# Kernel optimization log

Hardware: AMD Instinct MI355X
Metric: run time of the kernel (lower is better)

The kernel has to match this reference:

```python
import jax, jax.numpy as jnp
import numpy as np

B0 = 4
DIM = 128        # d_model / channels
D_INNER = 256    # expand * dim
D_STATE = 16
D_CONV = 4
DT_RANK = 8      # ceil(dim/16)
NSLICES = 16
IMG = (16, 24, 24)
EPS_LN = 1e-5    # nn.LayerNorm default
EPS_CF = 1e-6    # channels_first LayerNorm eps


def setup_inputs() -> dict:
    key = jax.random.key(0)
    ks = jax.random.split(key, 32)
    rn = lambda k, s, sc=1.0: jax.random.normal(k, s, jnp.float32) * sc
    inp = {"x": rn(ks[0], (B0, DIM) + IMG)}
    inp["ln_w"] = jnp.ones((DIM,), jnp.float32)
    inp["ln_b"] = jnp.zeros((DIM,), jnp.float32)
    inp["in_proj_w"] = rn(ks[1], (2 * D_INNER, DIM), 0.05)
    inp["out_proj_w"] = rn(ks[2], (DIM, D_INNER), 0.05)
    for i, sfx in enumerate(["f", "b", "s"]):
        b = 3 + i * 7
        inp[f"conv_w_{sfx}"] = rn(ks[b], (D_INNER, 1, D_CONV), 0.2)
        inp[f"conv_b_{sfx}"] = rn(ks[b + 1], (D_INNER,), 0.02)
        inp[f"xproj_w_{sfx}"] = rn(ks[b + 2], (DT_RANK + 2 * D_STATE, D_INNER), 0.05)
        inp[f"dtproj_w_{sfx}"] = rn(ks[b + 3], (D_INNER, DT_RANK), 0.1)
        inp[f"dtproj_b_{sfx}"] = rn(ks[b + 4], (D_INNER,), 0.1)
        # S4D-real-style init: A in [1, d_state]
        inp[f"A_log_{sfx}"] = jnp.log(jax.random.uniform(ks[b + 5], (D_INNER, D_STATE), jnp.float32, 1.0, 16.0))
        inp[f"D_{sfx}"] = jnp.ones((D_INNER,), jnp.float32)
    inp["nm_w"] = jnp.ones((DIM,), jnp.float32)
    inp["nm_b"] = jnp.zeros((DIM,), jnp.float32)
    return inp


def _mamba_inner(xz, conv_w, conv_b, xproj_w, dtproj_w, dtproj_b, A_log, Dp):
    """mamba_inner_fn_no_out_proj: xz (B, 2*d_inner, L) -> y (B, d_inner, L)."""
    d = conv_w.shape[0]
    x, z = xz[:, :d], xz[:, d:]
    # causal depthwise conv1d
    xc = jax.lax.conv_general_dilated(
        x, conv_w, (1,), [(conv_w.shape[-1] - 1, 0)],
        dimension_numbers=("NCH", "OIH", "NCH"), feature_group_count=d)
    xc = jax.nn.silu(xc + conv_b[None, :, None])
    x_dbl = jnp.einsum("bdl,rd->brl", xc, xproj_w)  # (B, R+2N, L)
    R = dtproj_w.shape[1]
    N = A_log.shape[1]
    dt = jax.nn.softplus(jnp.einsum("brl,dr->bdl", x_dbl[:, :R], dtproj_w) + dtproj_b[None, :, None])
    Bm, Cm = x_dbl[:, R:R + N], x_dbl[:, R + N:]
    A = -jnp.exp(A_log)  # (d, N)
    seq = (jnp.moveaxis(dt, -1, 0), jnp.moveaxis(xc, -1, 0),
           jnp.moveaxis(Bm, -1, 0), jnp.moveaxis(Cm, -1, 0))
    h0 = jnp.zeros((xz.shape[0], d, N), xz.dtype)

    def step(h, t):
        dt_t, u_t, B_t, C_t = t  # (B,d) (B,d) (B,N) (B,N)
        h = h * jnp.exp(dt_t[..., None] * A) + (dt_t * u_t)[..., None] * B_t[:, None, :]
        return h, jnp.einsum("bdn,bn->bd", h, C_t)

    _, ys = jax.lax.scan(step, h0, seq)  # ys: (L, B, d)
    y = jnp.moveaxis(ys, 0, -1) + Dp[None, :, None] * xc
    return y * jax.nn.silu(z)


def reference(x, ln_w, ln_b, in_proj_w, out_proj_w,
              conv_w_f, conv_b_f, xproj_w_f, dtproj_w_f, dtproj_b_f, A_log_f, D_f,
              conv_w_b, conv_b_b, xproj_w_b, dtproj_w_b, dtproj_b_b, A_log_b, D_b,
              conv_w_s, conv_b_s, xproj_w_s, dtproj_w_s, dtproj_b_s, A_log_s, D_s,
              nm_w, nm_b):
    B, C = x.shape[:2]
    img = x.shape[2:]
    L = int(np.prod(img))
    xf = jnp.transpose(x.reshape(B, C, L), (0, 2, 1))  # (B, L, C)
    # MambaLayer.norm (nn.LayerNorm over C)
    mu = xf.mean(-1, keepdims=True)
    var = ((xf - mu) ** 2).mean(-1, keepdims=True)
    xn = (xf - mu) / jnp.sqrt(var + EPS_LN) * ln_w + ln_b
    xz = jnp.einsum("blc,ec->bel", xn, in_proj_w)  # (B, 2*d_inner, L)
    # forward-direction scan
    out_f = _mamba_inner(xz, conv_w_f, conv_b_f, xproj_w_f, dtproj_w_f, dtproj_b_f, A_log_f, D_f)
    # backward-direction scan on flipped sequence, flipped back
    out_bw = jnp.flip(_mamba_inner(jnp.flip(xz, -1), conv_w_b, conv_b_b, xproj_w_b,
                                   dtproj_w_b, dtproj_b_b, A_log_b, D_b), -1)
    # slice-direction: torch chunk(nslices,-1) -> stack(-1) -> flatten(-2)
    ns, Lns = NSLICES, L // NSLICES
    xz_s = jnp.transpose(xz.reshape(B, 2 * D_INNER, ns, Lns), (0, 1, 3, 2)).reshape(B, 2 * D_INNER, L)
    out_s = _mamba_inner(xz_s, conv_w_s, conv_b_s, xproj_w_s, dtproj_w_s, dtproj_b_s, A_log_s, D_s)
    # torch: reshape(B,-1,ns,L//ns).permute(0,1,3,2).flatten(-2)
    out_s = jnp.transpose(out_s.reshape(B, D_INNER, ns, Lns), (0, 1, 3, 2)).reshape(B, D_INNER, L)
    y = jnp.einsum("bdl,cd->blc", out_f + out_bw + out_s, out_proj_w)  # out_proj, no bias
    x_mamba = jnp.transpose(y, (0, 2, 1)).reshape(x.shape) + x  # MambaLayer residual
    # SMBBlock: channels_first LayerNorm + residual
    mu2 = x_mamba.mean(1, keepdims=True)
    var2 = ((x_mamba - mu2) ** 2).mean(1, keepdims=True)
    bc = (C,) + (1,) * len(img)
    normed = nm_w.reshape(bc) * ((x_mamba - mu2) / jnp.sqrt(var2 + EPS_CF)) + nm_b.reshape(bc)
    return x_mamba + normed
```

## Files before the change

kernel.cpp:

```cpp
#include <hip/hip_runtime.h>

#define LSEQ 9216
#define CDIM 128
#define ED   512
#define DI   256
#define NST  16
#define NCH  512
#define CHL  18
#define SEG  32
#define LOG2E 1.44269504f
#define LN2  0.6931471805599453f

#if defined(__has_builtin)
#  if __has_builtin(__builtin_amdgcn_exp2f)
#    define FEXP2(x) __builtin_amdgcn_exp2f(x)
#  endif
#  if __has_builtin(__builtin_amdgcn_logf)
#    define FLOG2(x) __builtin_amdgcn_logf(x)
#  endif
#  if __has_builtin(__builtin_amdgcn_rcpf)
#    define FRCP(x) __builtin_amdgcn_rcpf(x)
#  endif
#endif
#ifndef FEXP2
#  define FEXP2(x) exp2f(x)
#endif
#ifndef FLOG2
#  define FLOG2(x) log2f(x)
#endif
#ifndef FRCP
#  define FRCP(x) (1.f / (x))
#endif

typedef __attribute__((ext_vector_type(8))) short short8v;
typedef __attribute__((ext_vector_type(4))) float float4v;

__device__ __forceinline__ float fsilu(float x) {
  return x * FRCP(1.f + FEXP2(-LOG2E * x));
}
__device__ __forceinline__ float fsoftplus(float x) {
  float sp = FLOG2(1.f + FEXP2(LOG2E * x)) * LN2;
  return (x > 20.f) ? x : sp;
}
__device__ __forceinline__ unsigned short f2bf(float f) {
  union { float f; unsigned u; } v; v.f = f;
  return (unsigned short)((v.u + 0x7FFFu + ((v.u >> 16) & 1u)) >> 16);
}
__device__ __forceinline__ float bf2f(unsigned short u) {
  union { unsigned u; float f; } v; v.u = ((unsigned)u) << 16;
  return v.f;
}
__device__ __forceinline__ int lmap(int p, int mode) {
  if (mode == 0) return p;
  if (mode == 1) return LSEQ - 1 - p;
  return (p & 15) * 576 + (p >> 4);
}

__global__ __launch_bounds__(256) void a2_kernel(
    const float* __restrict__ Af, const float* __restrict__ Ab,
    const float* __restrict__ As, float* __restrict__ A2) {
  int i = blockIdx.x * 256 + threadIdx.x;
  if (i >= 3 * DI * NST) return;
  int dir = i / (DI * NST), j = i % (DI * NST);
  const float* src = (dir == 0) ? Af : ((dir == 1) ? Ab : As);
  A2[i] = -expf(src[j]) * LOG2E;
}

__global__ __launch_bounds__(256) void wcast_kernel(
    const float* __restrict__ src, unsigned short* __restrict__ dst, int n) {
  int i = blockIdx.x * 256 + threadIdx.x;
  if (i < n) dst[i] = f2bf(src[i]);
}

__global__ __launch_bounds__(256) void ln_kernel(
    const float* __restrict__ x, const float* __restrict__ w,
    const float* __restrict__ bb, unsigned short* __restrict__ xn) {
  __shared__ float xt[CDIM][65];
  __shared__ float ps[4][64], pq[4][64];
  __shared__ float mu_s[64], rs_s[64];
  const int b = blockIdx.y, l0 = blockIdx.x * 64, tid = threadIdx.x;
  for (int idx = tid; idx < CDIM * 64; idx += 256) {
    int c = idx >> 6, ll = idx & 63;
    xt[c][ll] = x[((size_t)(b * CDIM + c)) * LSEQ + l0 + ll];
  }
  __syncthreads();
  {
    int ll = tid & 63, grp = tid >> 6;
    float s = 0.f, q = 0.f;
    for (int c = grp * 32; c < grp * 32 + 32; ++c) {
      float v = xt[c][ll]; s += v; q += v * v;
    }
    ps[grp][ll] = s; pq[grp][ll] = q;
  }
  __syncthreads();
  if (tid < 64) {
    float S = ps[0][tid] + ps[1][tid] + ps[2][tid] + ps[3][tid];
    float Q = pq[0][tid] + pq[1][tid] + pq[2][tid] + pq[3][tid];
    float mu = S * (1.f / 128.f);
    float var = Q * (1.f / 128.f) - mu * mu;
    mu_s[tid] = mu;
    rs_s[tid] = rsqrtf(var + 1e-5f);
  }
  __syncthreads();
  for (int idx = tid; idx < 64 * CDIM; idx += 256) {
    int c = idx & 127, ll = idx >> 7;
    float v = (xt[c][ll] - mu_s[ll]) * rs_s[ll] * w[c] + bb[c];
    xn[((size_t)(b * LSEQ + l0 + ll)) * CDIM + c] = f2bf(v);
  }
}

template <bool A_BF16, bool OUT_BF16>
__global__ __launch_bounds__(256) void gemm_mfma(
    const void* __restrict__ Ap, const unsigned short* __restrict__ Wb,
    void* __restrict__ Outp, int N, int K, int ldo) {
  __shared__ __align__(16) unsigned short As[64][40];
  __shared__ __align__(16) unsigned short Bs[128][40];
  const int tid = threadIdx.x;
  const int lane = tid & 63, wid = tid >> 6;
  const int wr = wid >> 1, wc = wid & 1;
  const int m0 = blockIdx.x * 64, n0 = blockIdx.y * 128;
  float4v acc[2][4];
#pragma unroll
  for (int s = 0; s < 2; ++s)
#pragma unroll
    for (int t = 0; t < 4; ++t)
#pragma unroll
      for (int r = 0; r < 4; ++r) acc[s][t][r] = 0.f;

  const int srow = tid >> 2, sslot = tid & 3;
  for (int k0 = 0; k0 < K; k0 += 32) {
    if constexpr (A_BF16) {
      const unsigned short* A = (const unsigned short*)Ap;
      *(short8v*)&As[srow][sslot * 8] =
          *(const short8v*)&A[(size_t)(m0 + srow) * K + k0 + sslot * 8];
    } else {
      const float* A = (const float*)Ap;
      const float4* src = (const float4*)&A[(size_t)(m0 + srow) * K + k0 + sslot * 8];
      float4 f0 = src[0], f1 = src[1];
      short8v v;
      v[0] = (short)f2bf(f0.x); v[1] = (short)f2bf(f0.y);
      v[2] = (short)f2bf(f0.z); v[3] = (short)f2bf(f0.w);
      v[4] = (short)f2bf(f1.x); v[5] = (short)f2bf(f1.y);
      v[6] = (short)f2bf(f1.z); v[7] = (short)f2bf(f1.w);
      *(short8v*)&As[srow][sslot * 8] = v;
    }
#pragma unroll
    for (int i = 0; i < 2; ++i) {
      int row = i * 64 + srow;
      int n = n0 + row;
      short8v v;
      if (n < N) {
        v = *(const short8v*)&Wb[(size_t)n * K + k0 + sslot * 8];
      } else {
#pragma unroll
        for (int q = 0; q < 8; ++q) v[q] = 0;
      }
      *(short8v*)&Bs[row][sslot * 8] = v;
    }
    __syncthreads();
    const int kk = (lane >> 4) * 8;
    const int mr = wr * 32 + (lane & 15);
    const int nr = wc * 64 + (lane & 15);
    short8v a_frag[2], b_frag[4];
#pragma unroll
    for (int s = 0; s < 2; ++s)
      a_frag[s] = *(const short8v*)&As[mr + s * 16][kk];
#pragma unroll
    for (int t = 0; t < 4; ++t)
      b_frag[t] = *(const short8v*)&Bs[nr + t * 16][kk];
#pragma unroll
    for (int s = 0; s < 2; ++s)
#pragma unroll
      for (int t = 0; t < 4; ++t)
        acc[s][t] = __builtin_amdgcn_mfma_f32_16x16x32_bf16(
            a_frag[s], b_frag[t], acc[s][t], 0, 0, 0);
    __syncthreads();
  }
  const int rbase = (lane >> 4) * 4;
  const int cbase = lane & 15;
#pragma unroll
  for (int s = 0; s < 2; ++s)
#pragma unroll
    for (int t = 0; t < 4; ++t) {
      int n = n0 + wc * 64 + t * 16 + cbase;
      if (n < N) {
#pragma unroll
        for (int r = 0; r < 4; ++r) {
          int m = m0 + wr * 32 + s * 16 + rbase + r;
          if constexpr (OUT_BF16)
            ((unsigned short*)Outp)[(size_t)m * ldo + n] = f2bf(acc[s][t][r]);
          else
            ((float*)Outp)[(size_t)m * ldo + n] = acc[s][t][r];
        }
      }
    }
}

template <int MODE>
__global__ __launch_bounds__(256) void conv_kernel(
    const unsigned short* __restrict__ xz, const float* __restrict__ cw,
    const float* __restrict__ cb, unsigned short* __restrict__ xc) {
  __shared__ float xs[67][64];
  const int p0 = blockIdx.x * 64, d0 = blockIdx.y * 64, b = blockIdx.z;
  const int tid = threadIdx.x;
  for (int idx = tid; idx < 67 * 32; idx += 256) {
    int pp = idx >> 5, dd2 = idx & 31;
    int q = p0 + pp - 3;
    float v0 = 0.f, v1 = 0.f;
    if (q >= 0) {
      int l = lmap(q, MODE);
      unsigned uu = *(const unsigned*)&xz[((size_t)b * LSEQ + l) * ED + d0 + dd2 * 2];
      union { unsigned u; float f; } a, c;
      a.u = (uu & 0xFFFFu) << 16;
      c.u = uu & 0xFFFF0000u;
      v0 = a.f; v1 = c.f;
    }
    xs[pp][dd2 * 2] = v0;
    xs[pp][dd2 * 2 + 1] = v1;
  }
  __syncthreads();
  const int dd = tid & 63, pg = tid >> 6;
  const int d = d0 + dd;
  const float w0 = cw[d * 4 + 0], w1 = cw[d * 4 + 1];
  const float w2 = cw[d * 4 + 2], w3 = cw[d * 4 + 3];
  const float bias = cb[d];
  for (int pp = pg * 16; pp < pg * 16 + 16; ++pp) {
    float acc = bias + w0 * xs[pp][dd] + w1 * xs[pp + 1][dd] +
                w2 * xs[pp + 2][dd] + w3 * xs[pp + 3][dd];
    xc[((size_t)b * LSEQ + p0 + pp) * DI + d] = f2bf(fsilu(acc));
  }
}

__global__ __launch_bounds__(256, 8) void scan_p1(
    const unsigned short* __restrict__ xc, const float* __restrict__ xdbl,
    const float* __restrict__ A2, const float* __restrict__ dtw,
    const float* __restrict__ dtbias, unsigned short* __restrict__ hout,
    float* __restrict__ dts) {
  __shared__ __align__(16) float Xl[CHL][24];
  const int c = blockIdx.x, b = blockIdx.y, d = threadIdx.x;
  const int p0 = c * CHL;
  for (int idx = d; idx < CHL * 24; idx += 256) {
    int pr = idx / 24, r = idx % 24;
    Xl[pr][r] = xdbl[((size_t)b * LSEQ + p0 + pr) * 40 + r];
  }
  float a2[NST], h[NST], dw[8];
  {
    const float4* A2v = (const float4*)(A2 + d * NST);
#pragma unroll
    for (int q = 0; q < 4; ++q) {
      float4 t = A2v[q];
      a2[q * 4 + 0] = t.x; a2[q * 4 + 1] = t.y;
      a2[q * 4 + 2] = t.z; a2[q * 4 + 3] = t.w;
    }
    const float4* Wv = (const float4*)(dtw + d * 8);
    float4 w0 = Wv[0], w1 = Wv[1];
    dw[0] = w0.x; dw[1] = w0.y; dw[2] = w0.z; dw[3] = w0.w;
    dw[4] = w1.x; dw[5] = w1.y; dw[6] = w1.z; dw[7] = w1.w;
  }
#pragma unroll
  for (int n = 0; n < NST; ++n) h[n] = 0.f;
  const float dbias = dtbias[d];
  float dtsum = 0.f;
  const unsigned short* up = xc + ((size_t)b * LSEQ + p0) * DI + d;
  __syncthreads();
  for (int pr = 0; pr < CHL; ++pr) {
    const float u = bf2f(*up); up += DI;
    const float4* Xr = (const float4*)Xl[pr];
    float4 x0 = Xr[0], x1 = Xr[1];
    float raw = dbias;
    raw = fmaf(dw[0], x0.x, raw); raw = fmaf(dw[1], x0.y, raw);
    raw = fmaf(dw[2], x0.z, raw); raw = fmaf(dw[3], x0.w, raw);
    raw = fmaf(dw[4], x1.x, raw); raw = fmaf(dw[5], x1.y, raw);
    raw = fmaf(dw[6], x1.z, raw); raw = fmaf(dw[7], x1.w, raw);
    const float dtv = fsoftplus(raw);
    const float dtu = dtv * u;
    dtsum += dtv;
    float4 b0 = Xr[2], b1 = Xr[3], b2 = Xr[4], b3 = Xr[5];
    const float Bv[16] = {b0.x, b0.y, b0.z, b0.w, b1.x, b1.y, b1.z, b1.w,
                          b2.x, b2.y, b2.z, b2.w, b3.x, b3.y, b3.z, b3.w};
#pragma unroll
    for (int n = 0; n < NST; ++n) {
      float a = FEXP2(dtv * a2[n]);
      h[n] = fmaf(h[n], a, dtu * Bv[n]);
    }
  }
  unsigned short* hb = hout + (((size_t)c * 4 + b) * DI + d) * NST;
  uint4 pk0, pk1;
  pk0.x = ((unsigned)f2bf(h[1]) << 16) | f2bf(h[0]);
  pk0.y = ((unsigned)f2bf(h[3]) << 16) | f2bf(h[2]);
  pk0.z = ((unsigned)f2bf(h[5]) << 16) | f2bf(h[4]);
  pk0.w = ((unsigned)f2bf(h[7]) << 16) | f2bf(h[6]);
  pk1.x = ((unsigned)f2bf(h[9]) << 16) | f2bf(h[8]);
  pk1.y = ((unsigned)f2bf(h[11]) << 16) | f2bf(h[10]);
  pk1.z = ((unsigned)f2bf(h[13]) << 16) | f2bf(h[12]);
  pk1.w = ((unsigned)f2bf(h[15]) << 16) | f2bf(h[14]);
  *(uint4*)hb = pk0;
  *(uint4*)(hb + 8) = pk1;
  dts[((size_t)c * 4 + b) * DI + d] = dtsum;
}

__global__ __launch_bounds__(256) void scan_p2a(
    unsigned short* __restrict__ hbuf, const float* __restrict__ dts,
    const float* __restrict__ A2, float* __restrict__ cumdts,
    float* __restrict__ segH, float* __restrict__ segdts) {
  const int s = blockIdx.x >> 4;
  const int rest = ((blockIdx.x & 15) << 8) + threadIdx.x;
  const int b = blockIdx.y;
  const int d = rest >> 4;
  const float a2 = A2[rest];
  const int c0 = s * SEG;
  float h = 0.f, cum = 0.f;
  float nh = bf2f(hbuf[((size_t)(c0 * 4 + b) << 12) + rest]);
  float nd = dts[(size_t)(c0 * 4 + b) * DI + d];
  for (int c = c0; c < c0 + SEG; ++c) {
    const float tmp = nh, dcur = nd;
    if (c + 1 < c0 + SEG) {
      nh = bf2f(hbuf[((size_t)((c + 1) * 4 + b) << 12) + rest]);
      nd = dts[(size_t)((c + 1) * 4 + b) * DI + d];
    }
    if ((rest & 15) == 0) cumdts[(size_t)(c * 4 + b) * DI + d] = cum;
    cum += dcur;
    hbuf[((size_t)(c * 4 + b) << 12) + rest] = f2bf(h);
    h = fmaf(FEXP2(dcur * a2), h, tmp);
  }
  segH[((size_t)(s * 4 + b) << 12) + rest] = h;
  if ((rest & 15) == 0) segdts[(size_t)(s * 4 + b) * DI + d] = cum;
}

__global__ __launch_bounds__(256) void scan_p2b(
    const float* __restrict__ segH, const float* __restrict__ segdts,
    const float* __restrict__ A2, float* __restrict__ segcarry) {
  const int g = blockIdx.x * 256 + threadIdx.x;
  const int b = g >> 12;
  const int rest = g & 4095;
  const int d = rest >> 4;
  const float a2 = A2[rest];
  float carry = 0.f;
#pragma unroll
  for (int s = 0; s < 16; ++s) {
    segcarry[((size_t)(s * 4 + b) << 12) + rest] = carry;
    const float decay = FEXP2(segdts[(size_t)(s * 4 + b) * DI + d] * a2);
    carry = fmaf(decay, carry, segH[((size_t)(s * 4 + b) << 12) + rest]);
  }
}

template <int MODE>
__global__ __launch_bounds__(256, 8) void scan_p3(
    const unsigned short* __restrict__ xc, const float* __restrict__ xdbl,
    const unsigned short* __restrict__ xz, const float* __restrict__ A2,
    const float* __restrict__ dtw, const float* __restrict__ dtbias,
    const unsigned short* __restrict__ hinit, const float* __restrict__ cumdts,
    const float* __restrict__ segcarry, const float* __restrict__ Dp,
    float* __restrict__ yacc) {
  __shared__ __align__(16) float Xl[CHL][40];
  const int c = blockIdx.x, b = blockIdx.y, d = threadIdx.x;
  const int p0 = c * CHL;
  for (int idx = d; idx < CHL * 40; idx += 256) {
    int pr = idx / 40, r = idx % 40;
    Xl[pr][r] = xdbl[((size_t)b * LSEQ + p0 + pr) * 40 + r];
  }
  float a2[NST], h[NST], dw[8];
  {
    const float4* A2v = (const float4*)(A2 + d * NST);
#pragma unroll
    for (int q = 0; q < 4; ++q) {
      float4 t = A2v[q];
      a2[q * 4 + 0] = t.x; a2[q * 4 + 1] = t.y;
      a2[q * 4 + 2] = t.z; a2[q * 4 + 3] = t.w;
    }
    const uint4* Hv = (const uint4*)(hinit + (((size_t)c * 4 + b) * DI + d) * NST);
    uint4 pa = Hv[0], pb = Hv[1];
    const unsigned pw[8] = {pa.x, pa.y, pa.z, pa.w, pb.x, pb.y, pb.z, pb.w};
#pragma unroll
    for (int j = 0; j < 8; ++j) {
      union { unsigned u; float f; } lo, hi;
      lo.u = (pw[j] & 0xFFFFu) << 16;
      hi.u = pw[j] & 0xFFFF0000u;
      h[2 * j] = lo.f; h[2 * j + 1] = hi.f;
    }
    const float cum = cumdts[((size_t)c * 4 + b) * DI + d];
    const float4* SC = (const float4*)(segcarry +
        (((size_t)(c / SEG) * 4 + b) << 12) + d * NST);
#pragma unroll
    for (int q = 0; q < 4; ++q) {
      float4 sc = SC[q];
      const float scv[4] = {sc.x, sc.y, sc.z, sc.w};
#pragma unroll
      for (int r = 0; r < 4; ++r) {
        int n = q * 4 + r;
        h[n] = fmaf(FEXP2(a2[n] * cum), scv[r], h[n]);
      }
    }
    const float4* Wv = (const float4*)(dtw + d * 8);
    float4 w0 = Wv[0], w1 = Wv[1];
    dw[0] = w0.x; dw[1] = w0.y; dw[2] = w0.z; dw[3] = w0.w;
    dw[4] = w1.x; dw[5] = w1.y; dw[6] = w1.z; dw[7] = w1.w;
  }
  const float dbias = dtbias[d];
  const float Dv = Dp[d];

  const unsigned short* up = xc + ((size_t)b * LSEQ + p0) * DI + d;
  const unsigned short* zp;
  float* op;
  ptrdiff_t zstride, ostride;
  if (MODE == 0) {
    zp = xz + ((size_t)b * LSEQ + p0) * ED + DI + d;              zstride = ED;
    op = yacc + ((size_t)b * LSEQ + p0) * DI + d;                 ostride = DI;
  } else if (MODE == 1) {
    zp = xz + ((size_t)b * LSEQ + (LSEQ - 1 - p0)) * ED + DI + d; zstride = -(ptrdiff_t)ED;
    op = yacc + ((size_t)b * LSEQ + (LSEQ - 1 - p0)) * DI + d;    ostride = -(ptrdiff_t)DI;
  } else {
    zp = nullptr; zstride = 0;
    const int lo0 = (p0 % 576) * 16 + p0 / 576;
    op = yacc + ((size_t)b * LSEQ + lo0) * DI + d;                ostride = 16 * DI;
  }
  __syncthreads();
  for (int pr = 0; pr < CHL; ++pr) {
    const float u = bf2f(*up); up += DI;
    const float4* Xr = (const float4*)Xl[pr];
    float4 x0 = Xr[0], x1 = Xr[1];
    float raw = dbias;
    raw = fmaf(dw[0], x0.x, raw); raw = fmaf(dw[1], x0.y, raw);
    raw = fmaf(dw[2], x0.z, raw); raw = fmaf(dw[3], x0.w, raw);
    raw = fmaf(dw[4], x1.x, raw); raw = fmaf(dw[5], x1.y, raw);
    raw = fmaf(dw[6], x1.z, raw); raw = fmaf(dw[7], x1.w, raw);
    const float dtv = fsoftplus(raw);
    const float dtu = dtv * u;
    float4 b0 = Xr[2], b1 = Xr[3], b2 = Xr[4], b3 = Xr[5];
    float4 c0 = Xr[6], c1 = Xr[7], c2 = Xr[8], c3 = Xr[9];
    const float Bv[16] = {b0.x, b0.y, b0.z, b0.w, b1.x, b1.y, b1.z, b1.w,
                          b2.x, b2.y, b2.z, b2.w, b3.x, b3.y, b3.z, b3.w};
    const float Cv[16] = {c0.x, c0.y, c0.z, c0.w, c1.x, c1.y, c1.z, c1.w,
                          c2.x, c2.y, c2.z, c2.w, c3.x, c3.y, c3.z, c3.w};
    float y0 = Dv * u, y1 = 0.f;
#pragma unroll
    for (int n = 0; n < NST; ++n) {
      float a = FEXP2(dtv * a2[n]);
      h[n] = fmaf(h[n], a, dtu * Bv[n]);
      if (n & 1) y1 = fmaf(h[n], Cv[n], y1);
      else       y0 = fmaf(h[n], Cv[n], y0);
    }
    float z;
    if (MODE == 2) {
      const int p = p0 + pr;
      const int lz = (p & 15) * 576 + (p >> 4);
      z = bf2f(xz[((size_t)b * LSEQ + lz) * ED + DI + d]);
    } else {
      z = bf2f(*zp); zp += zstride;
    }
    const float val = (y0 + y1) * fsilu(z);
    if (MODE == 0) *op = val;
    else           *op += val;
    op += ostride;
  }
}

__global__ __launch_bounds__(256) void final_kernel(
    const float* __restrict__ x, const float* __restrict__ yout,
    const float* __restrict__ nmw, const float* __restrict__ nmb,
    float* __restrict__ out) {
  __shared__ float xt[CDIM][65];
  __shared__ float ps[4][64], pq[4][64];
  __shared__ float mu_s[64], rs_s[64];
  const int b = blockIdx.y, l0 = blockIdx.x * 64, tid = threadIdx.x;
  for (int idx = tid; idx < CDIM * 64; idx += 256) {
    int c = idx >> 6, ll = idx & 63;
    xt[c][ll] = x[((size_t)(b * CDIM + c)) * LSEQ + l0 + ll];
  }
  __syncthreads();
  for (int idx = tid; idx < 64 * CDIM; idx += 256) {
    int c = idx & 127, ll = idx >> 7;
    xt[c][ll] += yout[((size_t)(b * LSEQ + l0 + ll)) * CDIM + c];
  }
  __syncthreads();
  {
    int ll = tid & 63, grp = tid >> 6;
    float s = 0.f, q = 0.f;
    for (int c = grp * 32; c < grp * 32 + 32; ++c) {
      float v = xt[c][ll]; s += v; q += v * v;
    }
    ps[grp][ll] = s; pq[grp][ll] = q;
  }
  __syncthreads();
  if (tid < 64) {
    float S = ps[0][tid] + ps[1][tid] + ps[2][tid] + ps[3][tid];
    float Q = pq[0][tid] + pq[1][tid] + pq[2][tid] + pq[3][tid];
    float mu = S * (1.f / 128.f);
    float var = Q * (1.f / 128.f) - mu * mu;
    mu_s[tid] = mu;
    rs_s[tid] = rsqrtf(var + 1e-6f);
  }
  __syncthreads();
  for (int idx = tid; idx < CDIM * 64; idx += 256) {
    int c = idx >> 6, ll = idx & 63;
    float v = xt[c][ll];
    float nv = v + nmw[c] * (v - mu_s[ll]) * rs_s[ll] + nmb[c];
    out[((size_t)(b * CDIM + c)) * LSEQ + l0 + ll] = nv;
  }
}

extern "C" void kernel_launch(void* const* d_in, const int* in_sizes, int n_in,
                              void* d_out, int out_size, void* d_ws, size_t ws_size,
                              hipStream_t stream) {
  (void)in_sizes; (void)n_in; (void)out_size;
  const float* x         = (const float*)d_in[0];
  const float* ln_w      = (const float*)d_in[1];
  const float* ln_b      = (const float*)d_in[2];
  const float* in_proj_w = (const float*)d_in[3];
  const float* out_projw = (const float*)d_in[4];
  const float* conv_w[3] = {(const float*)d_in[5],  (const float*)d_in[12], (const float*)d_in[19]};
  const float* conv_b[3] = {(const float*)d_in[6],  (const float*)d_in[13], (const float*)d_in[20]};
  const float* xproj[3]  = {(const float*)d_in[7],  (const float*)d_in[14], (const float*)d_in[21]};
  const float* dtw[3]    = {(const float*)d_in[8],  (const float*)d_in[15], (const float*)d_in[22]};
  const float* dtb[3]    = {(const float*)d_in[9],  (const float*)d_in[16], (const float*)d_in[23]};
  const float* alog[3]   = {(const float*)d_in[10], (const float*)d_in[17], (const float*)d_in[24]};
  const float* Dvec[3]   = {(const float*)d_in[11], (const float*)d_in[18], (const float*)d_in[25]};
  const float* nm_w      = (const float*)d_in[26];
  const float* nm_b      = (const float*)d_in[27];

  float* ws = (float*)d_ws;
  unsigned short* xn_us   = (unsigned short*)(ws);
  unsigned short* xz_us   = (unsigned short*)(ws + 2359296);
  unsigned short* xc_us   = (unsigned short*)(ws + 11796480);
  float* xdbl   = ws + 16515072;
  float* yacc   = ws + 17989632;
  float* yout   = ws + 27426816;
  float* A2     = ws + 32145408;
  unsigned short* wb = (unsigned short*)(ws + 32157696);
  unsigned short* hout_us = (unsigned short*)(ws + 32223232);
  float* dts      = ws + 36417536;
  float* cumdts   = ws + 36941824;
  float* segH     = ws + 37466112;
  float* segdts   = ws + 37728256;
  float* segcarry = ws + 37744640;
  if (ws_size < (size_t)38006784 * sizeof(float)) return;

  unsigned short* wb_in  = wb;
  unsigned short* wb_xp0 = wb + 65536;
  unsigned short* wb_xp1 = wb + 75776;
  unsigned short* wb_xp2 = wb + 86016;
  unsigned short* wb_out = wb + 96256;
  unsigned short* wb_xp[3] = {wb_xp0, wb_xp1, wb_xp2};

  a2_kernel<<<48, 256, 0, stream>>>(alog[0], alog[1], alog[2], A2);
  wcast_kernel<<<256, 256, 0, stream>>>(in_proj_w, wb_in, 65536);
  wcast_kernel<<<40, 256, 0, stream>>>(xproj[0], wb_xp0, 10240);
  wcast_kernel<<<40, 256, 0, stream>>>(xproj[1], wb_xp1, 10240);
  wcast_kernel<<<40, 256, 0, stream>>>(xproj[2], wb_xp2, 10240);
  wcast_kernel<<<128, 256, 0, stream>>>(out_projw, wb_out, 32768);

  ln_kernel<<<dim3(LSEQ / 64, 4), 256, 0, stream>>>(x, ln_w, ln_b, xn_us);
  gemm_mfma<true, true><<<dim3(576, 4), 256, 0, stream>>>(xn_us, wb_in, xz_us, 512, 128, 512);

  for (int dir = 0; dir < 3; ++dir) {
    if (dir == 0)
      conv_kernel<0><<<dim3(LSEQ / 64, 4, 4), 256, 0, stream>>>(xz_us, conv_w[0], conv_b[0], xc_us);
    else if (dir == 1)
      conv_kernel<1><<<dim3(LSEQ / 64, 4, 4), 256, 0, stream>>>(xz_us, conv_w[1], conv_b[1], xc_us);
    else
      conv_kernel<2><<<dim3(LSEQ / 64, 4, 4), 256, 0, stream>>>(xz_us, conv_w[2], conv_b[2], xc_us);

    gemm_mfma<true, false><<<dim3(576, 1), 256, 0, stream>>>(xc_us, wb_xp[dir], xdbl, 40, 256, 40);

    const float* A2d = A2 + dir * 4096;
    dim3 sg(NCH, 4);
    scan_p1<<<sg, 256, 0, stream>>>(xc_us, xdbl, A2d, dtw[dir], dtb[dir], hout_us, dts);
    scan_p2a<<<dim3(256, 4), 256, 0, stream>>>(hout_us, dts, A2d, cumdts, segH, segdts);
    scan_p2b<<<64, 256, 0, stream>>>(segH, segdts, A2d, segcarry);

    if (dir == 0)
      scan_p3<0><<<sg, 256, 0, stream>>>(xc_us, xdbl, xz_us, A2d, dtw[0], dtb[0],
                                         hout_us, cumdts, segcarry, Dvec[0], yacc);
    else if (dir == 1)
      scan_p3<1><<<sg, 256, 0, stream>>>(xc_us, xdbl, xz_us, A2d, dtw[1], dtb[1],
                                         hout_us, cumdts, segcarry, Dvec[1], yacc);
    else
      scan_p3<2><<<sg, 256, 0, stream>>>(xc_us, xdbl, xz_us, A2d, dtw[2], dtb[2],
                                         hout_us, cumdts, segcarry, Dvec[2], yacc);
  }
  gemm_mfma<false, false><<<dim3(576, 1), 256, 0, stream>>>(yacc, wb_out, yout, 128, 256, 128);
  final_kernel<<<dim3(LSEQ / 64, 4), 256, 0, stream>>>(x, yout, nm_w, nm_b, (float*)d_out);
}
```

Before: 481.7 us.

## Write per-direction scan outputs as bf16 and sum them inside out_proj GEMM

The three scan_p3 direction passes no longer read-modify-write a shared fp32 accumulator. Each now stores its gated output to its own bf16 buffer. A new specialised GEMM loads the three bf16 tiles, sums them in fp32, rounds to bf16 and runs MFMA against the out_proj weights. This removes the fp32 read-add-write traffic in two of the scan passes and the fp32 load in the final GEMM, at the cost of extra workspace and bf16 rounding of each partial output before summation.

```diff
diff --git a/kernel.cpp b/kernel.cpp
--- a/kernel.cpp
+++ b/kernel.cpp
@@ -196,6 +196,80 @@
     }
 }
 
+__global__ __launch_bounds__(256) void gemm_mfma3(
+    const unsigned short* __restrict__ yf, const unsigned short* __restrict__ yb,
+    const unsigned short* __restrict__ ys, const unsigned short* __restrict__ Wb,
+    float* __restrict__ Out) {
+  __shared__ __align__(16) unsigned short As[64][40];
+  __shared__ __align__(16) unsigned short Bs[128][40];
+  const int tid = threadIdx.x;
+  const int lane = tid & 63, wid = tid >> 6;
+  const int wr = wid >> 1, wc = wid & 1;
+  const int m0 = blockIdx.x * 64;
+  float4v acc[2][4];
+#pragma unroll
+  for (int s = 0; s < 2; ++s)
+#pragma unroll
+    for (int t = 0; t < 4; ++t)
+#pragma unroll
+      for (int r = 0; r < 4; ++r) acc[s][t][r] = 0.f;
+
+  const int srow = tid >> 2, sslot = tid & 3;
+  for (int k0 = 0; k0 < 256; k0 += 32) {
+    {
+      size_t base = (size_t)(m0 + srow) * DI + k0 + sslot * 8;
+      short8v vf = *(const short8v*)&yf[base];
+      short8v vb = *(const short8v*)&yb[base];
+      short8v vs = *(const short8v*)&ys[base];
+      short8v v;
+#pragma unroll
+      for (int q = 0; q < 8; ++q) {
+        float f = bf2f((unsigned short)vf[q]) + bf2f((unsigned short)vb[q]) +
+                  bf2f((unsigned short)vs[q]);
+        v[q] = (short)f2bf(f);
+      }
+      *(short8v*)&As[srow][sslot * 8] = v;
+    }
+#pragma unroll
+    for (int i = 0; i < 2; ++i) {
+      int row = i * 64 + srow;
+      *(short8v*)&Bs[row][sslot * 8] =
+          *(const short8v*)&Wb[(size_t)row * 256 + k0 + sslot * 8];
+    }
+    __syncthreads();
+    const int kk = (lane >> 4) * 8;
+    const int mr = wr * 32 + (lane & 15);
+    const int nr = wc * 64 + (lane & 15);
+    short8v a_frag[2], b_frag[4];
+#pragma unroll
+    for (int s = 0; s < 2; ++s)
+      a_frag[s] = *(const short8v*)&As[mr + s * 16][kk];
+#pragma unroll
+    for (int t = 0; t < 4; ++t)
+      b_frag[t] = *(const short8v*)&Bs[nr + t * 16][kk];
+#pragma unroll
+    for (int s = 0; s < 2; ++s)
+#pragma unroll
+      for (int t = 0; t < 4; ++t)
+        acc[s][t] = __builtin_amdgcn_mfma_f32_16x16x32_bf16(
+            a_frag[s], b_frag[t], acc[s][t], 0, 0, 0);
+    __syncthreads();
+  }
+  const int rbase = (lane >> 4) * 4;
+  const int cbase = lane & 15;
+#pragma unroll
+  for (int s = 0; s < 2; ++s)
+#pragma unroll
+    for (int t = 0; t < 4; ++t) {
+      int n = wc * 64 + t * 16 + cbase;
+#pragma unroll
+      for (int r = 0; r < 4; ++r) {
+        int m = m0 + wr * 32 + s * 16 + rbase + r;
+        Out[(size_t)m * CDIM + n] = acc[s][t][r];
+      }
+    }
+}
+
 template <int MODE>
 __global__ __launch_bounds__(256) void conv_kernel(
     const unsigned short* __restrict__ xz, const float* __restrict__ cw,
@@ -351,7 +425,7 @@
     const float* __restrict__ dtw, const float* __restrict__ dtbias,
     const unsigned short* __restrict__ hinit, const float* __restrict__ cumdts,
     const float* __restrict__ segcarry, const float* __restrict__ Dp,
-    float* __restrict__ yacc) {
+    unsigned short* __restrict__ ybuf) {
   __shared__ __align__(16) float Xl[CHL][40];
   const int c = blockIdx.x, b = blockIdx.y, d = threadIdx.x;
   const int p0 = c * CHL;
@@ -401,18 +475,18 @@
 
   const unsigned short* up = xc + ((size_t)b * LSEQ + p0) * DI + d;
   const unsigned short* zp;
-  float* op;
+  unsigned short* op;
   ptrdiff_t zstride, ostride;
   if (MODE == 0) {
     zp = xz + ((size_t)b * LSEQ + p0) * ED + DI + d;              zstride = ED;
-    op = yacc + ((size_t)b * LSEQ + p0) * DI + d;                 ostride = DI;
+    op = ybuf + ((size_t)b * LSEQ + p0) * DI + d;                 ostride = DI;
   } else if (MODE == 1) {
     zp = xz + ((size_t)b * LSEQ + (LSEQ - 1 - p0)) * ED + DI + d; zstride = -(ptrdiff_t)ED;
-    op = yacc + ((size_t)b * LSEQ + (LSEQ - 1 - p0)) * DI + d;    ostride = -(ptrdiff_t)DI;
+    op = ybuf + ((size_t)b * LSEQ + (LSEQ - 1 - p0)) * DI + d;    ostride = -(ptrdiff_t)DI;
   } else {
     zp = nullptr; zstride = 0;
     const int lo0 = (p0 % 576) * 16 + p0 / 576;
-    op = yacc + ((size_t)b * LSEQ + lo0) * DI + d;                ostride = 16 * DI;
+    op = ybuf + ((size_t)b * LSEQ + lo0) * DI + d;                ostride = 16 * DI;
   }
   __syncthreads();
   for (int pr = 0; pr < CHL; ++pr) {
@@ -448,9 +522,7 @@
     } else {
       z = bf2f(*zp); zp += zstride;
     }
-    const float val = (y0 + y1) * fsilu(z);
-    if (MODE == 0) *op = val;
-    else           *op += val;
+    *op = f2bf((y0 + y1) * fsilu(z));
     op += ostride;
   }
 }
@@ -523,17 +595,19 @@
   unsigned short* xz_us   = (unsigned short*)(ws + 2359296);
   unsigned short* xc_us   = (unsigned short*)(ws + 11796480);
   float* xdbl   = ws + 16515072;
-  float* yacc   = ws + 17989632;
-  float* yout   = ws + 27426816;
-  float* A2     = ws + 32145408;
-  unsigned short* wb = (unsigned short*)(ws + 32157696);
-  unsigned short* hout_us = (unsigned short*)(ws + 32223232);
-  float* dts      = ws + 36417536;
-  float* cumdts   = ws + 36941824;
-  float* segH     = ws + 37466112;
-  float* segdts   = ws + 37728256;
-  float* segcarry = ws + 37744640;
-  if (ws_size < (size_t)38006784 * sizeof(float)) return;
+  unsigned short* yf_us   = (unsigned short*)(ws + 17989632);
+  unsigned short* yb_us   = (unsigned short*)(ws + 22708224);
+  unsigned short* ys_us   = (unsigned short*)(ws + 27426816);
+  float* yout   = ws + 32145408;
+  float* A2     = ws + 36864000;
+  unsigned short* wb = (unsigned short*)(ws + 36876288);
+  unsigned short* hout_us = (unsigned short*)(ws + 36941824);
+  float* dts      = ws + 41136128;
+  float* cumdts   = ws + 41660416;
+  float* segH     = ws + 42184704;
+  float* segdts   = ws + 42446848;
+  float* segcarry = ws + 42463232;
+  if (ws_size < (size_t)42725376 * sizeof(float)) return;
 
   unsigned short* wb_in  = wb;
   unsigned short* wb_xp0 = wb + 65536;
@@ -541,6 +615,7 @@
   unsigned short* wb_xp2 = wb + 86016;
   unsigned short* wb_out = wb + 96256;
   unsigned short* wb_xp[3] = {wb_xp0, wb_xp1, wb_xp2};
+  unsigned short* ybuf[3] = {yf_us, yb_us, ys_us};
 
   a2_kernel<<<48, 256, 0, stream>>>(alog[0], alog[1], alog[2], A2);
   wcast_kernel<<<256, 256, 0, stream>>>(in_proj_w, wb_in, 65536);
@@ -570,14 +645,14 @@
 
     if (dir == 0)
       scan_p3<0><<<sg, 256, 0, stream>>>(xc_us, xdbl, xz_us, A2d, dtw[0], dtb[0],
-                                         hout_us, cumdts, segcarry, Dvec[0], yacc);
+                                         hout_us, cumdts, segcarry, Dvec[0], ybuf[0]);
     else if (dir == 1)
       scan_p3<1><<<sg, 256, 0, stream>>>(xc_us, xdbl, xz_us, A2d, dtw[1], dtb[1],
-                                         hout_us, cumdts, segcarry, Dvec[1], yacc);
+                                         hout_us, cumdts, segcarry, Dvec[1], ybuf[1]);
     else
       scan_p3<2><<<sg, 256, 0, stream>>>(xc_us, xdbl, xz_us, A2d, dtw[2], dtb[2],
-                                         hout_us, cumdts, segcarry, Dvec[2], yacc);
-  }
-  gemm_mfma<false, false><<<dim3(576, 1), 256, 0, stream>>>(yacc, wb_out, yout, 128, 256, 128);
+                                         hout_us, cumdts, segcarry, Dvec[2], ybuf[2]);
+  }
+  gemm_mfma3<<<576, 256, 0, stream>>>(yf_us, yb_us, ys_us, wb_out, yout);
   final_kernel<<<dim3(LSEQ / 64, 4), 256, 0, stream>>>(x, yout, nm_w, nm_b, (float*)d_out);
 }
```

Measured after the change: 452.9 us. -6.0%, faster.
